# Kernel tuning notes

Hardware: AMD Instinct MI355X
Metric: run time of the kernel (lower is better)

## Reference

```python
import jax, jax.numpy as jnp
import numpy as np

N_NODES = 20000
N_EDGES = 640000
NUM_FEATURES = 128
HIDDEN = 64
HEADS = 4
NUM_CLASSES = 16
NEG_SLOPE = 0.2  # PyG GATConv default leaky_relu slope


def gat_conv(x, src, dst, W, att_s, att_d, b, num_nodes, concat):
    """PyG-style GATConv (inference: attention dropout is identity).
    x: [N, F_in]; src/dst: [E] (self-loops already included);
    W: [F_in, H*C]; att_s/att_d: [H, C]; b: [H*C] or [C]."""
    H, C = att_s.shape
    h = (x @ W).reshape(num_nodes, H, C)            # [N,H,C]
    a_s = jnp.sum(h * att_s, axis=-1)               # [N,H]
    a_d = jnp.sum(h * att_d, axis=-1)               # [N,H]
    e = jax.nn.leaky_relu(a_s[src] + a_d[dst], NEG_SLOPE)  # [E,H]
    # softmax over incoming edges of each destination node
    emax = jax.ops.segment_max(e, dst, num_segments=num_nodes)  # [N,H]
    ex = jnp.exp(e - emax[dst])
    denom = jax.ops.segment_sum(ex, dst, num_segments=num_nodes)
    alpha = ex / denom[dst]                         # [E,H]
    msg = h[src] * alpha[..., None]                 # [E,H,C]
    out = jax.ops.segment_sum(msg, dst, num_segments=num_nodes)  # [N,H,C]
    out = out.reshape(num_nodes, H * C) if concat else out.mean(axis=1)
    return out + b


def setup_inputs() -> dict:
    key = jax.random.key(0)
    ks = jax.random.split(key, 12)
    d1_in, d1_out = NUM_FEATURES, HEADS * HIDDEN
    d2_in, d2_out = HEADS * HIDDEN, HEADS * HIDDEN
    return {
        "x": jax.random.normal(ks[0], (N_NODES, NUM_FEATURES), dtype=jnp.float32),
        "edge_index": jax.random.randint(ks[1], (2, N_EDGES), 0, N_NODES, dtype=jnp.int64)
        if jax.config.jax_enable_x64 else
        jax.random.randint(ks[1], (2, N_EDGES), 0, N_NODES, dtype=jnp.int32),
        "W1": jax.random.normal(ks[2], (d1_in, d1_out), dtype=jnp.float32) / np.sqrt(d1_in),
        "att_src1": jax.random.normal(ks[3], (HEADS, HIDDEN), dtype=jnp.float32) / np.sqrt(HIDDEN),
        "att_dst1": jax.random.normal(ks[4], (HEADS, HIDDEN), dtype=jnp.float32) / np.sqrt(HIDDEN),
        "b1": jnp.zeros((HEADS * HIDDEN,), dtype=jnp.float32),
        "W2": jax.random.normal(ks[5], (d2_in, d2_out), dtype=jnp.float32) / np.sqrt(d2_in),
        "att_src2": jax.random.normal(ks[6], (HEADS, HIDDEN), dtype=jnp.float32) / np.sqrt(HIDDEN),
        "att_dst2": jax.random.normal(ks[7], (HEADS, HIDDEN), dtype=jnp.float32) / np.sqrt(HIDDEN),
        "b2": jnp.zeros((HIDDEN,), dtype=jnp.float32),
        "Wout": jax.random.normal(ks[8], (HIDDEN, NUM_CLASSES), dtype=jnp.float32) / np.sqrt(HIDDEN),
        "bout": jnp.zeros((NUM_CLASSES,), dtype=jnp.float32),
    }


def reference(x, edge_index, W1, att_src1, att_dst1, b1, W2, att_src2, att_dst2, b2, Wout, bout):
    N = x.shape[0]
    loops = jnp.arange(N, dtype=edge_index.dtype)
    src = jnp.concatenate([edge_index[0], loops])   # PyG add_self_loops=True
    dst = jnp.concatenate([edge_index[1], loops])
    h = gat_conv(x, src, dst, W1, att_src1, att_dst1, b1, N, concat=True)
    h = jax.nn.elu(h)                               # dropout is identity at eval
    h = gat_conv(h, src, dst, W2, att_src2, att_dst2, b2, N, concat=False)
    return h @ Wout + bout
```

## Files before the change

### kernel.cpp

```cpp
#include <hip/hip_runtime.h>
#include <hip/hip_bf16.h>
#include <hip/hip_fp16.h>


#define HEADS 4
#define CDIM 64
#define HC 256
#define ELLW 96

typedef __attribute__((ext_vector_type(8))) short bf16x8;
typedef __attribute__((ext_vector_type(4))) float f32x4;

__device__ __forceinline__ short f32_to_bf16_rne(float v) {
  unsigned u = __float_as_uint(v);
  unsigned r = (u + 0x7FFFu + ((u >> 16) & 1u)) >> 16;
  return (short)r;
}
__device__ __forceinline__ float bf16_bits_to_f32(short s) {
  return __uint_as_float(((unsigned)(unsigned short)s) << 16);
}

__device__ __forceinline__ void fma_mix2(float& alo, float& ahi,
                                         unsigned reg, float ex) {
  asm("v_fma_mix_f32 %0, %2, %3, %0 op_sel:[0,0,0] op_sel_hi:[1,0,0]\n\t"
      "v_fma_mix_f32 %1, %2, %3, %1 op_sel:[1,0,0] op_sel_hi:[1,0,0]"
      : "+v"(alo), "+v"(ahi)
      : "v"(reg), "v"(ex));
}
__device__ __forceinline__ void fma_mix8(float ex, const uint4& u, float* acc) {
  fma_mix2(acc[0], acc[1], u.x, ex);
  fma_mix2(acc[2], acc[3], u.y, ex);
  fma_mix2(acc[4], acc[5], u.z, ex);
  fma_mix2(acc[6], acc[7], u.w, ex);
}

__global__ __launch_bounds__(256) void pack_w12_kernel(
    const float* __restrict__ W1, short* __restrict__ W1h,
    short* __restrict__ W1l, const float* __restrict__ W2,
    short* __restrict__ W2h, short* __restrict__ W2l) {
  const int i = blockIdx.x * 256 + threadIdx.x;
  if (i < 128 * 256) {
    const int k = i >> 8, n = i & 255;
    const float v = W1[i];
    const short hi = f32_to_bf16_rne(v);
    W1h[n * 128 + k] = hi;
    W1l[n * 128 + k] = f32_to_bf16_rne(v - bf16_bits_to_f32(hi));
  } else {
    const int j = i - 128 * 256;
    if (j >= 256 * 256) return;
    const int k = j >> 8, n = j & 255;
    const float v = W2[j];
    const short hi = f32_to_bf16_rne(v);
    W2h[n * 256 + k] = hi;
    W2l[n * 256 + k] = f32_to_bf16_rne(v - bf16_bits_to_f32(hi));
  }
}

__global__ __launch_bounds__(128) void gemm_mfma_split(
    const float* __restrict__ A, const short* __restrict__ Wt_hi,
    const short* __restrict__ Wt_lo, __half* __restrict__ h16,
    const float* __restrict__ att_s, const float* __restrict__ att_d,
    float* __restrict__ a_s, float* __restrict__ a_d, int M, int K) {
  __shared__ alignas(16) short As_hi[64 * 32];
  __shared__ alignas(16) short As_lo[64 * 32];
  const int t = threadIdx.x;
  const int wave = t >> 6;
  const int lane = t & 63;
  const int quad = lane >> 4;
  const int m16 = lane & 15;
  const int row0 = blockIdx.x * 64;
  const int col0 = blockIdx.y * 128 + wave * 64;
  const int head = col0 >> 6;

  f32x4 acc[4][4] = {};

  for (int k0 = 0; k0 < K; k0 += 32) {
    if (k0) __syncthreads();
#pragma unroll
    for (int uu = 0; uu < 2; ++uu) {
      const int u = t + uu * 128;
      const int r = u >> 2, seg = u & 3;
      const int gr = row0 + r;
      float vv[8] = {0.f, 0.f, 0.f, 0.f, 0.f, 0.f, 0.f, 0.f};
      if (gr < M) {
        const float* ap = A + (size_t)gr * K + k0 + seg * 8;
        const float4 v0 = *(const float4*)ap;
        const float4 v1 = *(const float4*)(ap + 4);
        vv[0] = v0.x; vv[1] = v0.y; vv[2] = v0.z; vv[3] = v0.w;
        vv[4] = v1.x; vv[5] = v1.y; vv[6] = v1.z; vv[7] = v1.w;
      }
      bf16x8 h8, l8;
#pragma unroll
      for (int j = 0; j < 8; ++j) {
        const short hi = f32_to_bf16_rne(vv[j]);
        h8[j] = hi;
        l8[j] = f32_to_bf16_rne(vv[j] - bf16_bits_to_f32(hi));
      }
      *(bf16x8*)(As_hi + r * 32 + seg * 8) = h8;
      *(bf16x8*)(As_lo + r * 32 + seg * 8) = l8;
    }
    bf16x8 b_hi[4], b_lo[4];
#pragma unroll
    for (int nt = 0; nt < 4; ++nt) {
      const size_t off = (size_t)(col0 + nt * 16 + m16) * K + k0 + quad * 8;
      b_hi[nt] = *(const bf16x8*)(Wt_hi + off);
      b_lo[nt] = *(const bf16x8*)(Wt_lo + off);
    }
    __syncthreads();
    bf16x8 a_hi[4], a_lo[4];
#pragma unroll
    for (int mt = 0; mt < 4; ++mt) {
      const int off = (mt * 16 + m16) * 32 + quad * 8;
      a_hi[mt] = *(const bf16x8*)(As_hi + off);
      a_lo[mt] = *(const bf16x8*)(As_lo + off);
    }
#pragma unroll
    for (int mt = 0; mt < 4; ++mt)
#pragma unroll
      for (int nt = 0; nt < 4; ++nt) {
        acc[mt][nt] = __builtin_amdgcn_mfma_f32_16x16x32_bf16(
            a_hi[mt], b_hi[nt], acc[mt][nt], 0, 0, 0);
        acc[mt][nt] = __builtin_amdgcn_mfma_f32_16x16x32_bf16(
            a_hi[mt], b_lo[nt], acc[mt][nt], 0, 0, 0);
        acc[mt][nt] = __builtin_amdgcn_mfma_f32_16x16x32_bf16(
            a_lo[mt], b_hi[nt], acc[mt][nt], 0, 0, 0);
      }
  }
  float sa[4], da[4];
#pragma unroll
  for (int nt = 0; nt < 4; ++nt) {
    sa[nt] = att_s[col0 + nt * 16 + m16];
    da[nt] = att_d[col0 + nt * 16 + m16];
  }
#pragma unroll
  for (int mt = 0; mt < 4; ++mt)
#pragma unroll
    for (int r = 0; r < 4; ++r) {
      const int gr = row0 + mt * 16 + quad * 4 + r;
      float ps = acc[mt][0][r] * sa[0] + acc[mt][1][r] * sa[1] +
                 acc[mt][2][r] * sa[2] + acc[mt][3][r] * sa[3];
      float pd = acc[mt][0][r] * da[0] + acc[mt][1][r] * da[1] +
                 acc[mt][2][r] * da[2] + acc[mt][3][r] * da[3];
#pragma unroll
      for (int off = 1; off <= 8; off <<= 1) {
        ps += __shfl_xor(ps, off);
        pd += __shfl_xor(pd, off);
      }
      if (gr < M) {
        if (m16 == 0) {
          a_s[gr * HEADS + head] = ps;
          a_d[gr * HEADS + head] = pd;
        }
#pragma unroll
        for (int nt = 0; nt < 4; ++nt)
          h16[(size_t)gr * HC + col0 + nt * 16 + m16] =
              __float2half(acc[mt][nt][r]);
      }
    }
}

__global__ __launch_bounds__(256) void ell_scatter_kernel(
    const int* __restrict__ src, const int* __restrict__ dst,
    int* __restrict__ cnt, int* __restrict__ ell, int E_raw, int Etot) {
  const int e = blockIdx.x * 256 + threadIdx.x;
  if (e >= Etot) return;
  const int s = (e < E_raw) ? src[e] : (e - E_raw);
  const int d = (e < E_raw) ? dst[e] : (e - E_raw);
  const int pos = atomicAdd(&cnt[d], 1);
  if (pos < ELLW) ell[d * ELLW + pos] = s;
}

__global__ __launch_bounds__(256) void gat_aggregate_kernel(
    const int* __restrict__ cnt, const int* __restrict__ ell,
    const __half* __restrict__ h16, const float* __restrict__ a_s,
    const float* __restrict__ a_d, const float* __restrict__ b,
    float* __restrict__ out, int mode) {
  const int bid = blockIdx.x;
  const int hd = bid & 3;
  const int n = (bid >> 2) * 4 + (threadIdx.x >> 6);
  const int lane = threadIdx.x & 63;
  const int q = lane >> 3;
  const int oc = lane & 7;
  const float ad = a_d[n * HEADS + hd];
  const int deg = cnt[n];
  const int* __restrict__ row = ell + n * ELLW;
  const char* hbase = (const char*)h16 + hd * 128 + oc * 16;
  const float* asb = a_s + hd;
  float acc[8] = {0.f, 0.f, 0.f, 0.f, 0.f, 0.f, 0.f, 0.f};
  float den = 0.f;
  int i = q;
  for (; i + 8 < deg; i += 16) {
    const int s0 = row[i];
    const int s1 = row[i + 8];
    const float as0 = asb[s0 * 4];
    const float as1 = asb[s1 * 4];
    const uint4 u0 = *(const uint4*)(hbase + ((unsigned)s0 << 9));
    const uint4 u1 = *(const uint4*)(hbase + ((unsigned)s1 << 9));
    float a0 = as0 + ad; a0 = fmaxf(a0, 0.2f * a0);
    float a1 = as1 + ad; a1 = fmaxf(a1, 0.2f * a1);
    const float e0 = __expf(a0);
    const float e1 = __expf(a1);
    den += e0 + e1;
    fma_mix8(e0, u0, acc);
    fma_mix8(e1, u1, acc);
  }
  for (; i < deg; i += 8) {
    const int s = row[i];
    float a = asb[s * 4] + ad;
    a = fmaxf(a, 0.2f * a);
    const float ex = __expf(a);
    den += ex;
    const uint4 u = *(const uint4*)(hbase + ((unsigned)s << 9));
    fma_mix8(ex, u, acc);
  }
#pragma unroll
  for (int off = 8; off <= 32; off <<= 1) {
#pragma unroll
    for (int k = 0; k < 8; ++k) acc[k] += __shfl_xor(acc[k], off);
    den += __shfl_xor(den, off);
  }
  if (lane < 8) {
    const float inv = 1.f / den;
    float u[8];
#pragma unroll
    for (int k = 0; k < 8; ++k) u[k] = acc[k] * inv;
    if (mode == 0) {
      const float* bb = b + hd * CDIM + oc * 8;
#pragma unroll
      for (int k = 0; k < 8; ++k) {
        const float t0 = u[k] + bb[k];
        u[k] = (t0 > 0.f) ? t0 : (__expf(t0) - 1.f);
      }
    }
    float* op = out + (size_t)n * HC + hd * CDIM + oc * 8;
    *(float4*)op = make_float4(u[0], u[1], u[2], u[3]);
    *(float4*)(op + 4) = make_float4(u[4], u[5], u[6], u[7]);
  }
}

__global__ __launch_bounds__(256) void final_fused_kernel(
    const float* __restrict__ agg, const float* __restrict__ b2,
    const float* __restrict__ Wout, const float* __restrict__ bout,
    float* __restrict__ out, int N) {
  const int n = blockIdx.x * 4 + (threadIdx.x >> 6);
  const int c = threadIdx.x & 63;
  if (n >= N) return;
  const float* ar = agg + (size_t)n * HC;
  const float m = 0.25f * (ar[c] + ar[c + 64] + ar[c + 128] + ar[c + 192]) +
                  b2[c];
  const float4* wr = (const float4*)(Wout + c * 16);
  const float4 w0 = wr[0], w1 = wr[1], w2 = wr[2], w3 = wr[3];
  float p[16] = {m * w0.x, m * w0.y, m * w0.z, m * w0.w,
                 m * w1.x, m * w1.y, m * w1.z, m * w1.w,
                 m * w2.x, m * w2.y, m * w2.z, m * w2.w,
                 m * w3.x, m * w3.y, m * w3.z, m * w3.w};
#pragma unroll
  for (int off = 1; off < 64; off <<= 1)
#pragma unroll
    for (int j = 0; j < 16; ++j) p[j] += __shfl_xor(p[j], off);
  if (c == 0) {
    float* op = out + (size_t)n * 16;
    *(float4*)op = make_float4(p[0] + bout[0], p[1] + bout[1],
                               p[2] + bout[2], p[3] + bout[3]);
    *(float4*)(op + 4) = make_float4(p[4] + bout[4], p[5] + bout[5],
                                     p[6] + bout[6], p[7] + bout[7]);
    *(float4*)(op + 8) = make_float4(p[8] + bout[8], p[9] + bout[9],
                                     p[10] + bout[10], p[11] + bout[11]);
    *(float4*)(op + 12) = make_float4(p[12] + bout[12], p[13] + bout[13],
                                      p[14] + bout[14], p[15] + bout[15]);
  }
}

extern "C" void kernel_launch(void* const* d_in, const int* in_sizes, int n_in,
                              void* d_out, int out_size, void* d_ws, size_t ws_size,
                              hipStream_t stream) {
  const float* x      = (const float*)d_in[0];
  const int*   eidx   = (const int*)d_in[1];
  const float* W1     = (const float*)d_in[2];
  const float* att_s1 = (const float*)d_in[3];
  const float* att_d1 = (const float*)d_in[4];
  const float* b1     = (const float*)d_in[5];
  const float* W2     = (const float*)d_in[6];
  const float* att_s2 = (const float*)d_in[7];
  const float* att_d2 = (const float*)d_in[8];
  const float* b2     = (const float*)d_in[9];
  const float* Wout   = (const float*)d_in[10];
  const float* bout   = (const float*)d_in[11];
  float* out          = (float*)d_out;

  const int N     = in_sizes[0] / 128;
  const int E_raw = in_sizes[1] / 2;
  const int Etot  = E_raw + N;
  const int* src = eidx;
  const int* dst = eidx + E_raw;

  float* ws = (float*)d_ws;
  float* buf_agg = ws;
  float* buf_as  = buf_agg + (size_t)N * HC;
  float* buf_ad  = buf_as + (size_t)N * HEADS;
  __half* h16    = (__half*)(buf_ad + (size_t)N * HEADS);
  int* cnt  = (int*)(h16 + (size_t)N * HC);
  int* ell  = cnt + N;
  uintptr_t wp = ((uintptr_t)(ell + (size_t)N * ELLW) + 15) & ~(uintptr_t)15;
  short* wt1_hi = (short*)wp;
  short* wt1_lo = wt1_hi + 256 * 128;
  short* wt2_hi = wt1_lo + 256 * 128;
  short* wt2_lo = wt2_hi + 256 * 256;

  const dim3 blk(256);
  const int g_edge = (Etot + 255) / 256;
  const dim3 g_gemm((N + 63) / 64, 2);
  const dim3 blk_gemm(128);

  pack_w12_kernel<<<(384 * 256 + 255) / 256, blk, 0, stream>>>(
      W1, wt1_hi, wt1_lo, W2, wt2_hi, wt2_lo);
  hipMemsetAsync(cnt, 0, (size_t)N * sizeof(int), stream);
  ell_scatter_kernel<<<g_edge, blk, 0, stream>>>(src, dst, cnt, ell, E_raw, Etot);

  gemm_mfma_split<<<g_gemm, blk_gemm, 0, stream>>>(
      x, wt1_hi, wt1_lo, h16, att_s1, att_d1, buf_as, buf_ad, N, 128);
  gat_aggregate_kernel<<<N, blk, 0, stream>>>(cnt, ell, h16, buf_as,
                                              buf_ad, b1, buf_agg, 0);

  gemm_mfma_split<<<g_gemm, blk_gemm, 0, stream>>>(
      buf_agg, wt2_hi, wt2_lo, h16, att_s2, att_d2, buf_as, buf_ad, N, 256);
  gat_aggregate_kernel<<<N, blk, 0, stream>>>(cnt, ell, h16, buf_as,
                                              buf_ad, b2, buf_agg, 1);

  final_fused_kernel<<<(N + 3) / 4, blk, 0, stream>>>(buf_agg, b2, Wout, bout,
                                                      out, N);
}
```

Baseline: 269.5 us.

## Remap GAT aggregation to one wave per node covering all heads

The aggregation kernel now assigns one wavefront per destination node, with each lane owning four channels across all heads, instead of one wave per node-head split over edge groups. Each neighbor's full fp16 feature row is fetched as one coalesced load, and the cross-lane shuffle reduction is removed. Edges are processed in unrolled batches of eight with clamped indices and masked weights to keep several gathers in flight. The tradeoff is serial iteration over the degree within each wave, plus padded reads of unused ELL slots.

```diff
diff --git a/kernel.cpp b/kernel.cpp
--- a/kernel.cpp
+++ b/kernel.cpp
@@ -26,12 +26,6 @@
       "v_fma_mix_f32 %1, %2, %3, %1 op_sel:[1,0,0] op_sel_hi:[1,0,0]"
       : "+v"(alo), "+v"(ahi)
       : "v"(reg), "v"(ex));
-}
-__device__ __forceinline__ void fma_mix8(float ex, const uint4& u, float* acc) {
-  fma_mix2(acc[0], acc[1], u.x, ex);
-  fma_mix2(acc[2], acc[3], u.y, ex);
-  fma_mix2(acc[4], acc[5], u.z, ex);
-  fma_mix2(acc[6], acc[7], u.w, ex);
 }
 
 __global__ __launch_bounds__(256) void pack_w12_kernel(
@@ -174,68 +168,56 @@
     const int* __restrict__ cnt, const int* __restrict__ ell,
     const __half* __restrict__ h16, const float* __restrict__ a_s,
     const float* __restrict__ a_d, const float* __restrict__ b,
-    float* __restrict__ out, int mode) {
-  const int bid = blockIdx.x;
-  const int hd = bid & 3;
-  const int n = (bid >> 2) * 4 + (threadIdx.x >> 6);
+    float* __restrict__ out, int N, int mode) {
+  const int nn = __builtin_amdgcn_readfirstlane(
+      blockIdx.x * 4 + (threadIdx.x >> 6));
+  if (nn >= N) return;
   const int lane = threadIdx.x & 63;
-  const int q = lane >> 3;
-  const int oc = lane & 7;
-  const float ad = a_d[n * HEADS + hd];
-  const int deg = cnt[n];
-  const int* __restrict__ row = ell + n * ELLW;
-  const char* hbase = (const char*)h16 + hd * 128 + oc * 16;
-  const float* asb = a_s + hd;
-  float acc[8] = {0.f, 0.f, 0.f, 0.f, 0.f, 0.f, 0.f, 0.f};
-  float den = 0.f;
-  int i = q;
-  for (; i + 8 < deg; i += 16) {
-    const int s0 = row[i];
-    const int s1 = row[i + 8];
-    const float as0 = asb[s0 * 4];
-    const float as1 = asb[s1 * 4];
-    const uint4 u0 = *(const uint4*)(hbase + ((unsigned)s0 << 9));
-    const uint4 u1 = *(const uint4*)(hbase + ((unsigned)s1 << 9));
-    float a0 = as0 + ad; a0 = fmaxf(a0, 0.2f * a0);
-    float a1 = as1 + ad; a1 = fmaxf(a1, 0.2f * a1);
-    const float e0 = __expf(a0);
-    const float e1 = __expf(a1);
-    den += e0 + e1;
-    fma_mix8(e0, u0, acc);
-    fma_mix8(e1, u1, acc);
-  }
-  for (; i < deg; i += 8) {
-    const int s = row[i];
-    float a = asb[s * 4] + ad;
-    a = fmaxf(a, 0.2f * a);
-    const float ex = __expf(a);
-    den += ex;
-    const uint4 u = *(const uint4*)(hbase + ((unsigned)s << 9));
-    fma_mix8(ex, u, acc);
-  }
-#pragma unroll
-  for (int off = 8; off <= 32; off <<= 1) {
-#pragma unroll
-    for (int k = 0; k < 8; ++k) acc[k] += __shfl_xor(acc[k], off);
-    den += __shfl_xor(den, off);
-  }
-  if (lane < 8) {
-    const float inv = 1.f / den;
-    float u[8];
-#pragma unroll
-    for (int k = 0; k < 8; ++k) u[k] = acc[k] * inv;
-    if (mode == 0) {
-      const float* bb = b + hd * CDIM + oc * 8;
-#pragma unroll
-      for (int k = 0; k < 8; ++k) {
-        const float t0 = u[k] + bb[k];
-        u[k] = (t0 > 0.f) ? t0 : (__expf(t0) - 1.f);
-      }
-    }
-    float* op = out + (size_t)n * HC + hd * CDIM + oc * 8;
-    *(float4*)op = make_float4(u[0], u[1], u[2], u[3]);
-    *(float4*)(op + 4) = make_float4(u[4], u[5], u[6], u[7]);
-  }
+  const int hd = lane >> 4;
+  const float ad = a_d[nn * HEADS + hd];
+  const int deg = __builtin_amdgcn_readfirstlane(cnt[nn]);
+  const int* __restrict__ rowp = ell + nn * ELLW;
+  const unsigned nclamp = (unsigned)(N - 1);
+  const char* __restrict__ hby = (const char*)h16;
+  const unsigned lo8 = (unsigned)lane * 8u;
+  float acc0 = 0.f, acc1 = 0.f, acc2 = 0.f, acc3 = 0.f, den = 0.f;
+
+  for (int j0 = 0; j0 < deg; j0 += 8) {
+    unsigned su[8];
+#pragma unroll
+    for (int j = 0; j < 8; ++j) {
+      const unsigned s = (unsigned)rowp[j0 + j];
+      su[j] = (s > nclamp) ? nclamp : s;
+    }
+    float asv[8];
+    uint2 hv[8];
+#pragma unroll
+    for (int j = 0; j < 8; ++j) {
+      asv[j] = a_s[su[j] * HEADS + hd];
+      hv[j] = *(const uint2*)(hby + (((size_t)su[j]) << 9) + lo8);
+    }
+#pragma unroll
+    for (int j = 0; j < 8; ++j) {
+      float a = asv[j] + ad;
+      a = fmaxf(a, 0.2f * a);
+      const float ex = (j0 + j < deg) ? __expf(a) : 0.f;
+      den += ex;
+      fma_mix2(acc0, acc1, hv[j].x, ex);
+      fma_mix2(acc2, acc3, hv[j].y, ex);
+    }
+  }
+
+  const float inv = 1.f / den;
+  float u0 = acc0 * inv, u1 = acc1 * inv, u2 = acc2 * inv, u3 = acc3 * inv;
+  if (mode == 0) {
+    const float4 bb = *(const float4*)(b + lane * 4);
+    u0 += bb.x; u1 += bb.y; u2 += bb.z; u3 += bb.w;
+    u0 = (u0 > 0.f) ? u0 : (__expf(u0) - 1.f);
+    u1 = (u1 > 0.f) ? u1 : (__expf(u1) - 1.f);
+    u2 = (u2 > 0.f) ? u2 : (__expf(u2) - 1.f);
+    u3 = (u3 > 0.f) ? u3 : (__expf(u3) - 1.f);
+  }
+  *(float4*)(out + (size_t)nn * HC + lane * 4) = make_float4(u0, u1, u2, u3);
 }
 
 __global__ __launch_bounds__(256) void final_fused_kernel(
@@ -311,6 +293,7 @@
   const int g_edge = (Etot + 255) / 256;
   const dim3 g_gemm((N + 63) / 64, 2);
   const dim3 blk_gemm(128);
+  const int g_agg = (N + 3) / 4;
 
   pack_w12_kernel<<<(384 * 256 + 255) / 256, blk, 0, stream>>>(
       W1, wt1_hi, wt1_lo, W2, wt2_hi, wt2_lo);
@@ -319,13 +302,13 @@
 
   gemm_mfma_split<<<g_gemm, blk_gemm, 0, stream>>>(
       x, wt1_hi, wt1_lo, h16, att_s1, att_d1, buf_as, buf_ad, N, 128);
-  gat_aggregate_kernel<<<N, blk, 0, stream>>>(cnt, ell, h16, buf_as,
-                                              buf_ad, b1, buf_agg, 0);
+  gat_aggregate_kernel<<<g_agg, blk, 0, stream>>>(cnt, ell, h16, buf_as,
+                                                  buf_ad, b1, buf_agg, N, 0);
 
   gemm_mfma_split<<<g_gemm, blk_gemm, 0, stream>>>(
       buf_agg, wt2_hi, wt2_lo, h16, att_s2, att_d2, buf_as, buf_ad, N, 256);
-  gat_aggregate_kernel<<<N, blk, 0, stream>>>(cnt, ell, h16, buf_as,
-                                              buf_ad, b2, buf_agg, 1);
+  gat_aggregate_kernel<<<g_agg, blk, 0, stream>>>(cnt, ell, h16, buf_as,
+                                                  buf_ad, b2, buf_agg, N, 1);
 
   final_fused_kernel<<<(N + 3) / 4, blk, 0, stream>>>(buf_agg, b2, Wout, bout,
                                                       out, N);
```

New measurement: 267.2 us. About the same (-0.9%).
